# Optimization experiments

Measured on AMD Instinct MI355X. Metric: run time of the kernel, lower is better.

Reference implementation:

```python
import jax, jax.numpy as jnp
import numpy as np

B, D, O, E, H, K = 4096, 1024, 1024, 8, 4096, 2


def setup_inputs() -> dict:
    key = jax.random.key(0)
    ks = jax.random.split(key, 5)
    scale_g = 1.0 / np.sqrt(D)
    scale_1 = 1.0 / np.sqrt(D)
    scale_2 = 1.0 / np.sqrt(H)
    return {
        "x": jax.random.normal(ks[0], (B, D), jnp.float32),
        "gate_w": jax.random.normal(ks[1], (D, E), jnp.float32) * scale_g,
        "gate_b": jnp.zeros((E,), jnp.float32),
        "w1": jax.random.normal(ks[2], (E, D, H), jnp.float32) * scale_1,
        "b1": jnp.zeros((E, H), jnp.float32),
        "w2": jax.random.normal(ks[3], (E, H, O), jnp.float32) * scale_2,
        "b2": jnp.zeros((E, O), jnp.float32),
    }


def reference(x, gate_w, gate_b, w1, b1, w2, b2):
    # Router: top-k logits, softmax over the k selected logits only
    logits = x @ gate_w + gate_b                      # [B, E]
    top_vals, top_idx = jax.lax.top_k(logits, K)      # [B, K]
    routing_w = jax.nn.softmax(top_vals, axis=-1)     # [B, K]

    # Dense all-expert MLP (grouped GEMM), then gather the k selected outputs
    h = jax.nn.relu(jnp.einsum("bd,edh->beh", x, w1) + b1)  # [B, E, H]
    y = jnp.einsum("beh,eho->beo", h, w2) + b2              # [B, E, O]
    sel = jnp.take_along_axis(y, top_idx[:, :, None], axis=1)  # [B, K, O]
    return jnp.sum(routing_w[:, :, None] * sel, axis=1)        # [B, O]
```

## Files before the change

kernel.cpp:

```cpp
#include <hip/hip_runtime.h>
#include <stdint.h>

typedef short bf16x8 __attribute__((ext_vector_type(8)));
typedef float f32x4  __attribute__((ext_vector_type(4)));

constexpr int BT = 4096;
constexpr int DD = 1024;
constexpr int OO = 1024;
constexpr int EE = 8;
constexpr int HH = 4096;
constexpr int SLOTS = 2 * BT;

constexpr int BM = 256, BN = 128, BK = 32;
constexpr int RING = 4;
constexpr int A_USH = BM * BK;
constexpr int TILE_USH = (BM + BN) * BK;
constexpr int MAXT = 40;

__device__ __forceinline__ unsigned short f2bf(float f) {
  unsigned u = __float_as_uint(f);
  u += 0x7fffu + ((u >> 16) & 1u);
  return (unsigned short)(u >> 16);
}

__device__ __forceinline__ void glds16(const unsigned short* g, unsigned short* l) {
  __builtin_amdgcn_global_load_lds(
      (const __attribute__((address_space(1))) void*)g,
      (__attribute__((address_space(3))) void*)l, 16, 0, 0);
}

__global__ __launch_bounds__(256) void router_k(const float* __restrict__ x,
                                                const float* __restrict__ gw,
                                                const float* __restrict__ gb,
                                                unsigned short* __restrict__ xb,
                                                int* __restrict__ cnt,
                                                int* __restrict__ list,
                                                float* __restrict__ rw) {
  int wave = threadIdx.x >> 6, lane = threadIdx.x & 63;
  int b = blockIdx.x * 4 + wave;
  const float* xrow = x + (size_t)b * DD;
  float acc[8];
#pragma unroll
  for (int e = 0; e < 8; ++e) acc[e] = 0.f;
#pragma unroll
  for (int i = 0; i < 4; ++i) {
    int d0 = i * 256 + lane * 4;
    float4 v = *(const float4*)&xrow[d0];
    unsigned lo = (unsigned)f2bf(v.x) | ((unsigned)f2bf(v.y) << 16);
    unsigned hi = (unsigned)f2bf(v.z) | ((unsigned)f2bf(v.w) << 16);
    *(uint2*)&xb[(size_t)b * DD + d0] = make_uint2(lo, hi);
    const float* g0 = &gw[(size_t)d0 * 8];
    float fv[4] = {v.x, v.y, v.z, v.w};
#pragma unroll
    for (int q = 0; q < 4; ++q) {
      float4 ga = *(const float4*)&g0[q * 8];
      float4 gc = *(const float4*)&g0[q * 8 + 4];
      acc[0] += fv[q] * ga.x; acc[1] += fv[q] * ga.y;
      acc[2] += fv[q] * ga.z; acc[3] += fv[q] * ga.w;
      acc[4] += fv[q] * gc.x; acc[5] += fv[q] * gc.y;
      acc[6] += fv[q] * gc.z; acc[7] += fv[q] * gc.w;
    }
  }
#pragma unroll
  for (int off = 32; off > 0; off >>= 1) {
#pragma unroll
    for (int e = 0; e < 8; ++e) acc[e] += __shfl_down(acc[e], off);
  }
  if (lane == 0) {
    float v[8];
#pragma unroll
    for (int e = 0; e < 8; ++e) v[e] = acc[e] + gb[e];
    int i0 = 0;
#pragma unroll
    for (int e = 1; e < 8; ++e) if (v[e] > v[i0]) i0 = e;
    int i1 = (i0 == 0) ? 1 : 0;
#pragma unroll
    for (int e = 0; e < 8; ++e) if (e != i0 && v[e] > v[i1]) i1 = e;
    float e1 = __expf(v[i1] - v[i0]);
    float inv = 1.0f / (1.0f + e1);
    int p0 = atomicAdd(&cnt[i0], 1);
    list[i0 * BT + p0] = 2 * b;     rw[2 * b]     = inv;
    int p1 = atomicAdd(&cnt[i1], 1);
    list[i1 * BT + p1] = 2 * b + 1; rw[2 * b + 1] = e1 * inv;
  }
}

__global__ void tilemap_k(const int* __restrict__ cnt, int* __restrict__ tmap,
                          int* __restrict__ ntiles) {
  if (threadIdx.x == 0 && blockIdx.x == 0) {
    int t = 0, basewalk = 0;
    for (int e = 0; e < EE; ++e) {
      int c = cnt[e];
      for (int m0 = 0; m0 < c; m0 += BM) {
        tmap[4 * t] = e; tmap[4 * t + 1] = m0; tmap[4 * t + 2] = basewalk + m0; ++t;
      }
      basewalk += c;
    }
    *ntiles = t;
  }
}

__global__ __launch_bounds__(256) void cvt_t_k(const float* __restrict__ src,
                                               unsigned short* __restrict__ dst,
                                               int R, int C) {
  __shared__ unsigned short tile[64][66];
  int e = blockIdx.z;
  const float* s = src + (size_t)e * R * C;
  unsigned short* d = dst + (size_t)e * R * C;
  int r0 = blockIdx.x << 6, c0 = blockIdx.y << 6;
  int t = threadIdx.x;
#pragma unroll
  for (int p = 0; p < 4; ++p) {
    int ch = p * 256 + t;
    int rr = ch >> 4, cc = (ch & 15) << 2;
    float4 v = *(const float4*)&s[(size_t)(r0 + rr) * C + c0 + cc];
    unsigned lo = (unsigned)f2bf(v.x) | ((unsigned)f2bf(v.y) << 16);
    unsigned hi = (unsigned)f2bf(v.z) | ((unsigned)f2bf(v.w) << 16);
    *(uint2*)&tile[rr][cc] = make_uint2(lo, hi);
  }
  __syncthreads();
#pragma unroll
  for (int p = 0; p < 4; ++p) {
    int ch = p * 256 + t;
    int cc = ch >> 4, rr = (ch & 15) << 2;
    unsigned short v0 = tile[rr + 0][cc];
    unsigned short v1 = tile[rr + 1][cc];
    unsigned short v2 = tile[rr + 2][cc];
    unsigned short v3 = tile[rr + 3][cc];
    unsigned lo = (unsigned)v0 | ((unsigned)v1 << 16);
    unsigned hi = (unsigned)v2 | ((unsigned)v3 << 16);
    *(uint2*)&d[(size_t)(c0 + cc) * R + r0 + rr] = make_uint2(lo, hi);
  }
}

__global__ __launch_bounds__(512, 2) void gemm1_k(const unsigned short* __restrict__ xb,
                                                  const unsigned short* __restrict__ w1t,
                                                  const float* __restrict__ b1,
                                                  const int* __restrict__ cnt,
                                                  const int* __restrict__ list,
                                                  const int* __restrict__ tmap,
                                                  const int* __restrict__ ntiles,
                                                  unsigned short* __restrict__ hc) {
  int ti = blockIdx.y;
  if (ti >= *ntiles) return;
  int e = tmap[4 * ti], m0 = tmap[4 * ti + 1], base = tmap[4 * ti + 2];
  int cnt_e = cnt[e];
  int n0 = blockIdx.x * BN;

  __shared__ int slotbuf[BM];
  __shared__ __align__(16) unsigned short lds[RING * TILE_USH];

  int t = threadIdx.x;
  if (t < BM) {
    int r = m0 + t;
    slotbuf[t] = list[e * BT + (r < cnt_e ? r : 0)];
  }
  __syncthreads();

  int w = t >> 6, l = t & 63, lm = l & 15, lq = l >> 4;
  int wr = w >> 1, wc = w & 1;

  int rstage = t >> 2;
  int ch8 = (t & 3) * 8;
  const unsigned short* aS0 = xb + (size_t)(slotbuf[rstage] >> 1) * DD + ch8;
  const unsigned short* aS1 = xb + (size_t)(slotbuf[128 + rstage] >> 1) * DD + ch8;
  const unsigned short* bS  = w1t + (size_t)e * HH * DD + (size_t)(n0 + rstage) * DD + ch8;
  int dA0 = w * 512, dA1 = 4096 + w * 512, dB = A_USH + w * 512;

  int afo[4], bfo[4];
#pragma unroll
  for (int mi = 0; mi < 4; ++mi) afo[mi] = (wr * 64 + mi * 16 + lm) * BK + lq * 8;
#pragma unroll
  for (int ni = 0; ni < 4; ++ni) bfo[ni] = A_USH + (wc * 64 + ni * 16 + lm) * BK + lq * 8;

  f32x4 acc[4][4];
#pragma unroll
  for (int mi = 0; mi < 4; ++mi)
#pragma unroll
    for (int ni = 0; ni < 4; ++ni) acc[mi][ni] = f32x4{0.f, 0.f, 0.f, 0.f};

  constexpr int NT = DD / BK;

#pragma unroll
  for (int p = 0; p < RING - 1; ++p) {
    unsigned short* Lb = lds + p * TILE_USH;
    glds16(aS0 + p * BK, Lb + dA0);
    glds16(aS1 + p * BK, Lb + dA1);
    glds16(bS  + p * BK, Lb + dB);
  }
  asm volatile("s_waitcnt vmcnt(6)" ::: "memory");
  __builtin_amdgcn_s_barrier();
  asm volatile("" ::: "memory");

  for (int tt = 0; tt < NT; ++tt) {
    const unsigned short* Lc = lds + (tt & 3) * TILE_USH;
    bf16x8 af[4], bf[4];
#pragma unroll
    for (int mi = 0; mi < 4; ++mi) af[mi] = *(const bf16x8*)&Lc[afo[mi]];
#pragma unroll
    for (int ni = 0; ni < 4; ++ni) bf[ni] = *(const bf16x8*)&Lc[bfo[ni]];
    {
      int ts = tt + 3;
      int ko = (ts < NT ? ts : NT - 1) * BK;
      unsigned short* Lb = lds + (ts & 3) * TILE_USH;
      glds16(aS0 + ko, Lb + dA0);
      glds16(aS1 + ko, Lb + dA1);
      glds16(bS  + ko, Lb + dB);
    }
    __builtin_amdgcn_s_setprio(1);
#pragma unroll
    for (int mi = 0; mi < 4; ++mi)
#pragma unroll
      for (int ni = 0; ni < 4; ++ni)
        acc[mi][ni] = __builtin_amdgcn_mfma_f32_16x16x32_bf16(af[mi], bf[ni], acc[mi][ni], 0, 0, 0);
    __builtin_amdgcn_s_setprio(0);
    asm volatile("s_waitcnt vmcnt(6)" ::: "memory");
    __builtin_amdgcn_s_barrier();
    asm volatile("" ::: "memory");
  }

  asm volatile("s_waitcnt vmcnt(0)" ::: "memory");
  __builtin_amdgcn_s_barrier();
  asm volatile("" ::: "memory");
  unsigned short* cb = lds + w * 4096;
  float bias[4];
#pragma unroll
  for (int ni = 0; ni < 4; ++ni) bias[ni] = b1[e * HH + n0 + wc * 64 + ni * 16 + lm];
#pragma unroll
  for (int mi = 0; mi < 4; ++mi)
#pragma unroll
    for (int ni = 0; ni < 4; ++ni)
#pragma unroll
      for (int r = 0; r < 4; ++r)
        cb[(mi * 16 + lq * 4 + r) * 64 + ni * 16 + lm] =
            f2bf(fmaxf(acc[mi][ni][r] + bias[ni], 0.0f));
  asm volatile("s_waitcnt lgkmcnt(0)" ::: "memory");
#pragma unroll
  for (int it = 0; it < 8; ++it) {
    int rr = it * 8 + (l >> 3), chk = l & 7;
    int lrow = wr * 64 + rr;
    if (m0 + lrow < cnt_e) {
      uint4 v = *(const uint4*)&cb[rr * 64 + chk * 8];
      *(uint4*)&hc[(size_t)(base + lrow) * HH + n0 + wc * 64 + chk * 8] = v;
    }
  }
}

__global__ __launch_bounds__(512, 2) void gemm2_k(const unsigned short* __restrict__ hc,
                                                  const unsigned short* __restrict__ w2t,
                                                  const float* __restrict__ b2,
                                                  const int* __restrict__ cnt,
                                                  const int* __restrict__ list,
                                                  const int* __restrict__ tmap,
                                                  const int* __restrict__ ntiles,
                                                  const float* __restrict__ rw,
                                                  float* __restrict__ ybuf,
                                                  float* __restrict__ out) {
  int ti = blockIdx.y;
  if (ti >= *ntiles) return;
  int e = tmap[4 * ti], m0 = tmap[4 * ti + 1], base = tmap[4 * ti + 2];
  int cnt_e = cnt[e];
  int n0 = blockIdx.x * BN;
  int z = blockIdx.z;
  int ksl = HH / gridDim.z;
  int kb0 = z * ksl;
  int NT = ksl / BK;

  __shared__ int slotbuf[BM];
  __shared__ float rwbuf[BM];
  __shared__ __align__(16) unsigned short lds[RING * TILE_USH];

  int t = threadIdx.x;
  if (t < BM) {
    int r = m0 + t;
    int s_ = list[e * BT + (r < cnt_e ? r : 0)];
    slotbuf[t] = s_;
    rwbuf[t] = rw[s_];
  }
  __syncthreads();

  int w = t >> 6, l = t & 63, lm = l & 15, lq = l >> 4;
  int wr = w >> 1, wc = w & 1;

  int rstage = t >> 2, ch8 = (t & 3) * 8;
  int gr0 = base + rstage;       if (gr0 > SLOTS - 1) gr0 = SLOTS - 1;
  int gr1 = base + 128 + rstage; if (gr1 > SLOTS - 1) gr1 = SLOTS - 1;
  const unsigned short* aS0 = hc + (size_t)gr0 * HH + kb0 + ch8;
  const unsigned short* aS1 = hc + (size_t)gr1 * HH + kb0 + ch8;
  const unsigned short* bS  = w2t + (size_t)e * OO * HH + (size_t)(n0 + rstage) * HH + kb0 + ch8;
  int dA0 = w * 512, dA1 = 4096 + w * 512, dB = A_USH + w * 512;

  int afo[4], bfo[4];
#pragma unroll
  for (int mi = 0; mi < 4; ++mi) afo[mi] = (wr * 64 + mi * 16 + lm) * BK + lq * 8;
#pragma unroll
  for (int ni = 0; ni < 4; ++ni) bfo[ni] = A_USH + (wc * 64 + ni * 16 + lm) * BK + lq * 8;

  f32x4 acc[4][4];
#pragma unroll
  for (int mi = 0; mi < 4; ++mi)
#pragma unroll
    for (int ni = 0; ni < 4; ++ni) acc[mi][ni] = f32x4{0.f, 0.f, 0.f, 0.f};

#pragma unroll
  for (int p = 0; p < RING - 1; ++p) {
    unsigned short* Lb = lds + p * TILE_USH;
    glds16(aS0 + p * BK, Lb + dA0);
    glds16(aS1 + p * BK, Lb + dA1);
    glds16(bS  + p * BK, Lb + dB);
  }
  asm volatile("s_waitcnt vmcnt(6)" ::: "memory");
  __builtin_amdgcn_s_barrier();
  asm volatile("" ::: "memory");

  for (int tt = 0; tt < NT; ++tt) {
    const unsigned short* Lc = lds + (tt & 3) * TILE_USH;
    bf16x8 af[4], bf[4];
#pragma unroll
    for (int mi = 0; mi < 4; ++mi) af[mi] = *(const bf16x8*)&Lc[afo[mi]];
#pragma unroll
    for (int ni = 0; ni < 4; ++ni) bf[ni] = *(const bf16x8*)&Lc[bfo[ni]];
    {
      int ts = tt + 3;
      int ko = (ts < NT ? ts : NT - 1) * BK;
      unsigned short* Lb = lds + (ts & 3) * TILE_USH;
      glds16(aS0 + ko, Lb + dA0);
      glds16(aS1 + ko, Lb + dA1);
      glds16(bS  + ko, Lb + dB);
    }
    __builtin_amdgcn_s_setprio(1);
#pragma unroll
    for (int mi = 0; mi < 4; ++mi)
#pragma unroll
      for (int ni = 0; ni < 4; ++ni)
        acc[mi][ni] = __builtin_amdgcn_mfma_f32_16x16x32_bf16(af[mi], bf[ni], acc[mi][ni], 0, 0, 0);
    __builtin_amdgcn_s_setprio(0);
    asm volatile("s_waitcnt vmcnt(6)" ::: "memory");
    __builtin_amdgcn_s_barrier();
    asm volatile("" ::: "memory");
  }

  bool addb = (z == 0);
  size_t ybase = (size_t)z * SLOTS;
#pragma unroll
  for (int ni = 0; ni < 4; ++ni) {
    int ncol = n0 + wc * 64 + ni * 16 + lm;
    float bias = addb ? b2[e * OO + ncol] : 0.0f;
#pragma unroll
    for (int mi = 0; mi < 4; ++mi)
#pragma unroll
      for (int r = 0; r < 4; ++r) {
        int lrow = wr * 64 + mi * 16 + lq * 4 + r;
        if (m0 + lrow < cnt_e) {
          float v = (acc[mi][ni][r] + bias) * rwbuf[lrow];
          int slot = slotbuf[lrow];
          if (ybuf) ybuf[(ybase + slot) * OO + ncol] = v;
          else      atomicAdd(&out[(size_t)(slot >> 1) * OO + ncol], v);
        }
      }
  }
}

__global__ __launch_bounds__(256) void combine_k(const float* __restrict__ y,
                                                 float* __restrict__ out, int nz) {
  int i = blockIdx.x * 256 + threadIdx.x;
  int b = i >> 8, c = i & 255;
  f32x4 acc = {0.f, 0.f, 0.f, 0.f};
  for (int z = 0; z < nz; ++z) {
#pragma unroll
    for (int k = 0; k < 2; ++k) {
      const float4 v = *(const float4*)&y[((size_t)z * SLOTS + 2 * b + k) * OO + c * 4];
      acc[0] += v.x; acc[1] += v.y; acc[2] += v.z; acc[3] += v.w;
    }
  }
  *(f32x4*)&out[(size_t)b * OO + c * 4] = acc;
}

extern "C" void kernel_launch(void* const* d_in, const int* in_sizes, int n_in,
                              void* d_out, int out_size, void* d_ws, size_t ws_size,
                              hipStream_t stream) {
  const float* x  = (const float*)d_in[0];
  const float* gw = (const float*)d_in[1];
  const float* gb = (const float*)d_in[2];
  const float* w1 = (const float*)d_in[3];
  const float* b1 = (const float*)d_in[4];
  const float* w2 = (const float*)d_in[5];
  const float* b2 = (const float*)d_in[6];
  float* out = (float*)d_out;
  char* ws = (char*)d_ws;

  int*            cnt    = (int*)(ws);
  int*            ntiles = (int*)(ws + 64);
  int*            tmap   = (int*)(ws + 128);
  float*          rw     = (float*)(ws + 4096);
  int*            list   = (int*)(ws + (64u << 10));
  unsigned short* xb     = (unsigned short*)(ws + (1u  << 20));
  unsigned short* wt     = (unsigned short*)(ws + (9u  << 20));
  unsigned short* hc     = (unsigned short*)(ws + (73u << 20));
  float*          ybuf   = (float*)(ws + (138u << 20));

  size_t need_min = (138u << 20);
  if (ws_size < need_min) return;
  int zsplit;
  float* ypass;
  if (ws_size >= (138u << 20) + (size_t)2 * SLOTS * OO * 4) { zsplit = 2; ypass = ybuf; }
  else if (ws_size >= (138u << 20) + (size_t)SLOTS * OO * 4) { zsplit = 1; ypass = ybuf; }
  else { zsplit = 2; ypass = nullptr; }

  hipMemsetAsync(cnt, 0, 64, stream);
  if (!ypass) hipMemsetAsync(out, 0, (size_t)BT * OO * sizeof(float), stream);

  router_k<<<BT / 4, 256, 0, stream>>>(x, gw, gb, xb, cnt, list, rw);
  tilemap_k<<<1, 64, 0, stream>>>(cnt, tmap, ntiles);
  cvt_t_k<<<dim3(DD / 64, HH / 64, EE), 256, 0, stream>>>(w1, wt, DD, HH);
  gemm1_k<<<dim3(HH / BN, MAXT), 512, 0, stream>>>(xb, wt, b1, cnt, list, tmap, ntiles, hc);
  cvt_t_k<<<dim3(HH / 64, OO / 64, EE), 256, 0, stream>>>(w2, wt, HH, OO);
  gemm2_k<<<dim3(OO / BN, MAXT, zsplit), 512, 0, stream>>>(hc, wt, b2, cnt, list, tmap, ntiles, rw, ypass, out);
  if (ypass)
    combine_k<<<BT * OO / 1024, 256, 0, stream>>>(ybuf, out, zsplit);
}
```

Baseline: 683.2 us.

## Widen GEMM tiles to 256x256 with XOR-swizzled LDS and reordered prefetch

Both grouped GEMM kernels grow the N tile from 128 to 256, so each warp now computes a 128x64 sub-tile (8x4 MFMAs) in a 2x4 warp grid. This raises arithmetic intensity per LDS byte and per global load. LDS chunks are XOR-swizzled on both the global_load_lds write side and the fragment read side to cut bank conflicts, and the next-stage prefetch is now issued before the fragment reads. The cost is higher register pressure from 128 accumulator floats per lane, larger LDS use, and fewer blocks in the grid. Host launch grid dimensions presumably have to change for the wider tile, and that part is not shown.

Result: slower. 733.8 us (+7.4%).

```diff
diff --git a/kernel.cpp b/kernel.cpp
--- a/kernel.cpp
+++ b/kernel.cpp
@@ -11,10 +11,10 @@
 constexpr int HH = 4096;
 constexpr int SLOTS = 2 * BT;
 
-constexpr int BM = 256, BN = 128, BK = 32;
+constexpr int BM = 256, BN = 256, BK = 32;
 constexpr int RING = 4;
 constexpr int A_USH = BM * BK;
-constexpr int TILE_USH = (BM + BN) * BK;
+constexpr int SLOT_USH = (BM + BN) * BK;
 constexpr int MAXT = 40;
 
 __device__ __forceinline__ unsigned short f2bf(float f) {
@@ -148,7 +148,7 @@
   int n0 = blockIdx.x * BN;
 
   __shared__ int slotbuf[BM];
-  __shared__ __align__(16) unsigned short lds[RING * TILE_USH];
+  __shared__ __align__(16) unsigned short lds[RING * SLOT_USH];
 
   int t = threadIdx.x;
   if (t < BM) {
@@ -158,24 +158,31 @@
   __syncthreads();
 
   int w = t >> 6, l = t & 63, lm = l & 15, lq = l >> 4;
-  int wr = w >> 1, wc = w & 1;
-
-  int rstage = t >> 2;
-  int ch8 = (t & 3) * 8;
-  const unsigned short* aS0 = xb + (size_t)(slotbuf[rstage] >> 1) * DD + ch8;
-  const unsigned short* aS1 = xb + (size_t)(slotbuf[128 + rstage] >> 1) * DD + ch8;
-  const unsigned short* bS  = w1t + (size_t)e * HH * DD + (size_t)(n0 + rstage) * DD + ch8;
-  int dA0 = w * 512, dA1 = 4096 + w * 512, dB = A_USH + w * 512;
-
-  int afo[4], bfo[4];
-#pragma unroll
-  for (int mi = 0; mi < 4; ++mi) afo[mi] = (wr * 64 + mi * 16 + lm) * BK + lq * 8;
-#pragma unroll
-  for (int ni = 0; ni < 4; ++ni) bfo[ni] = A_USH + (wc * 64 + ni * 16 + lm) * BK + lq * 8;
-
-  f32x4 acc[4][4];
-#pragma unroll
-  for (int mi = 0; mi < 4; ++mi)
+  int wr = w >> 2, wc = w & 3;
+
+  const unsigned short* aS[2];
+  const unsigned short* bS[2];
+  int dA[2], dB[2];
+#pragma unroll
+  for (int j = 0; j < 2; ++j) {
+    int row = j * 128 + w * 16 + (l >> 2);
+    int sch = ((l & 3) ^ ((row >> 1) & 3)) * 8;
+    aS[j] = xb + (size_t)(slotbuf[row] >> 1) * DD + sch;
+    bS[j] = w1t + (size_t)e * HH * DD + (size_t)(n0 + row) * DD + sch;
+    dA[j] = j * 4096 + w * 512;
+    dB[j] = A_USH + j * 4096 + w * 512;
+  }
+
+  int xc = lq ^ ((lm >> 1) & 3);
+  int afo[8], bfo[4];
+#pragma unroll
+  for (int mi = 0; mi < 8; ++mi) afo[mi] = (wr * 128 + mi * 16 + lm) * BK + xc * 8;
+#pragma unroll
+  for (int ni = 0; ni < 4; ++ni) bfo[ni] = A_USH + (wc * 64 + ni * 16 + lm) * BK + xc * 8;
+
+  f32x4 acc[8][4];
+#pragma unroll
+  for (int mi = 0; mi < 8; ++mi)
 #pragma unroll
     for (int ni = 0; ni < 4; ++ni) acc[mi][ni] = f32x4{0.f, 0.f, 0.f, 0.f};
 
@@ -183,38 +190,40 @@
 
 #pragma unroll
   for (int p = 0; p < RING - 1; ++p) {
-    unsigned short* Lb = lds + p * TILE_USH;
-    glds16(aS0 + p * BK, Lb + dA0);
-    glds16(aS1 + p * BK, Lb + dA1);
-    glds16(bS  + p * BK, Lb + dB);
-  }
-  asm volatile("s_waitcnt vmcnt(6)" ::: "memory");
+    unsigned short* Lb = lds + p * SLOT_USH;
+    glds16(aS[0] + p * BK, Lb + dA[0]);
+    glds16(aS[1] + p * BK, Lb + dA[1]);
+    glds16(bS[0] + p * BK, Lb + dB[0]);
+    glds16(bS[1] + p * BK, Lb + dB[1]);
+  }
+  asm volatile("s_waitcnt vmcnt(8)" ::: "memory");
   __builtin_amdgcn_s_barrier();
   asm volatile("" ::: "memory");
 
   for (int tt = 0; tt < NT; ++tt) {
-    const unsigned short* Lc = lds + (tt & 3) * TILE_USH;
-    bf16x8 af[4], bf[4];
-#pragma unroll
-    for (int mi = 0; mi < 4; ++mi) af[mi] = *(const bf16x8*)&Lc[afo[mi]];
-#pragma unroll
-    for (int ni = 0; ni < 4; ++ni) bf[ni] = *(const bf16x8*)&Lc[bfo[ni]];
     {
       int ts = tt + 3;
       int ko = (ts < NT ? ts : NT - 1) * BK;
-      unsigned short* Lb = lds + (ts & 3) * TILE_USH;
-      glds16(aS0 + ko, Lb + dA0);
-      glds16(aS1 + ko, Lb + dA1);
-      glds16(bS  + ko, Lb + dB);
-    }
+      unsigned short* Lb = lds + (ts & 3) * SLOT_USH;
+      glds16(aS[0] + ko, Lb + dA[0]);
+      glds16(aS[1] + ko, Lb + dA[1]);
+      glds16(bS[0] + ko, Lb + dB[0]);
+      glds16(bS[1] + ko, Lb + dB[1]);
+    }
+    const unsigned short* Lc = lds + (tt & 3) * SLOT_USH;
+    bf16x8 af[8], bf[4];
+#pragma unroll
+    for (int mi = 0; mi < 8; ++mi) af[mi] = *(const bf16x8*)&Lc[afo[mi]];
+#pragma unroll
+    for (int ni = 0; ni < 4; ++ni) bf[ni] = *(const bf16x8*)&Lc[bfo[ni]];
     __builtin_amdgcn_s_setprio(1);
 #pragma unroll
-    for (int mi = 0; mi < 4; ++mi)
+    for (int mi = 0; mi < 8; ++mi)
 #pragma unroll
       for (int ni = 0; ni < 4; ++ni)
         acc[mi][ni] = __builtin_amdgcn_mfma_f32_16x16x32_bf16(af[mi], bf[ni], acc[mi][ni], 0, 0, 0);
     __builtin_amdgcn_s_setprio(0);
-    asm volatile("s_waitcnt vmcnt(6)" ::: "memory");
+    asm volatile("s_waitcnt vmcnt(8)" ::: "memory");
     __builtin_amdgcn_s_barrier();
     asm volatile("" ::: "memory");
   }
@@ -222,12 +231,12 @@
   asm volatile("s_waitcnt vmcnt(0)" ::: "memory");
   __builtin_amdgcn_s_barrier();
   asm volatile("" ::: "memory");
-  unsigned short* cb = lds + w * 4096;
+  unsigned short* cb = lds + w * 8192;
   float bias[4];
 #pragma unroll
   for (int ni = 0; ni < 4; ++ni) bias[ni] = b1[e * HH + n0 + wc * 64 + ni * 16 + lm];
 #pragma unroll
-  for (int mi = 0; mi < 4; ++mi)
+  for (int mi = 0; mi < 8; ++mi)
 #pragma unroll
     for (int ni = 0; ni < 4; ++ni)
 #pragma unroll
@@ -236,12 +245,12 @@
             f2bf(fmaxf(acc[mi][ni][r] + bias[ni], 0.0f));
   asm volatile("s_waitcnt lgkmcnt(0)" ::: "memory");
 #pragma unroll
-  for (int it = 0; it < 8; ++it) {
+  for (int it = 0; it < 16; ++it) {
     int rr = it * 8 + (l >> 3), chk = l & 7;
-    int lrow = wr * 64 + rr;
-    if (m0 + lrow < cnt_e) {
+    int grow = wr * 128 + rr;
+    if (m0 + grow < cnt_e) {
       uint4 v = *(const uint4*)&cb[rr * 64 + chk * 8];
-      *(uint4*)&hc[(size_t)(base + lrow) * HH + n0 + wc * 64 + chk * 8] = v;
+      *(uint4*)&hc[(size_t)(base + grow) * HH + n0 + wc * 64 + chk * 8] = v;
     }
   }
 }
@@ -268,7 +277,7 @@
 
   __shared__ int slotbuf[BM];
   __shared__ float rwbuf[BM];
-  __shared__ __align__(16) unsigned short lds[RING * TILE_USH];
+  __shared__ __align__(16) unsigned short lds[RING * SLOT_USH];
 
   int t = threadIdx.x;
   if (t < BM) {
@@ -280,65 +289,75 @@
   __syncthreads();
 
   int w = t >> 6, l = t & 63, lm = l & 15, lq = l >> 4;
-  int wr = w >> 1, wc = w & 1;
-
-  int rstage = t >> 2, ch8 = (t & 3) * 8;
-  int gr0 = base + rstage;       if (gr0 > SLOTS - 1) gr0 = SLOTS - 1;
-  int gr1 = base + 128 + rstage; if (gr1 > SLOTS - 1) gr1 = SLOTS - 1;
-  const unsigned short* aS0 = hc + (size_t)gr0 * HH + kb0 + ch8;
-  const unsigned short* aS1 = hc + (size_t)gr1 * HH + kb0 + ch8;
-  const unsigned short* bS  = w2t + (size_t)e * OO * HH + (size_t)(n0 + rstage) * HH + kb0 + ch8;
-  int dA0 = w * 512, dA1 = 4096 + w * 512, dB = A_USH + w * 512;
-
-  int afo[4], bfo[4];
-#pragma unroll
-  for (int mi = 0; mi < 4; ++mi) afo[mi] = (wr * 64 + mi * 16 + lm) * BK + lq * 8;
-#pragma unroll
-  for (int ni = 0; ni < 4; ++ni) bfo[ni] = A_USH + (wc * 64 + ni * 16 + lm) * BK + lq * 8;
-
-  f32x4 acc[4][4];
-#pragma unroll
-  for (int mi = 0; mi < 4; ++mi)
+  int wr = w >> 2, wc = w & 3;
+
+  const unsigned short* aS[2];
+  const unsigned short* bS[2];
+  int dA[2], dB[2];
+#pragma unroll
+  for (int j = 0; j < 2; ++j) {
+    int row = j * 128 + w * 16 + (l >> 2);
+    int sch = ((l & 3) ^ ((row >> 1) & 3)) * 8;
+    int gr = base + row; if (gr > SLOTS - 1) gr = SLOTS - 1;
+    aS[j] = hc + (size_t)gr * HH + kb0 + sch;
+    bS[j] = w2t + (size_t)e * OO * HH + (size_t)(n0 + row) * HH + kb0 + sch;
+    dA[j] = j * 4096 + w * 512;
+    dB[j] = A_USH + j * 4096 + w * 512;
+  }
+
+  int xc = lq ^ ((lm >> 1) & 3);
+  int afo[8], bfo[4];
+#pragma unroll
+  for (int mi = 0; mi < 8; ++mi) afo[mi] = (wr * 128 + mi * 16 + lm) * BK + xc * 8;
+#pragma unroll
+  for (int ni = 0; ni < 4; ++ni) bfo[ni] = A_USH + (wc * 64 + ni * 16 + lm) * BK + xc * 8;
+
+  f32x4 acc[8][4];
+#pragma unroll
+  for (int mi = 0; mi < 8; ++mi)
 #pragma unroll
     for (int ni = 0; ni < 4; ++ni) acc[mi][ni] = f32x4{0.f, 0.f, 0.f, 0.f};
 
 #pragma unroll
   for (int p = 0; p < RING - 1; ++p) {
-    unsigned short* Lb = lds + p * TILE_USH;
-    glds16(aS0 + p * BK, Lb + dA0);
-    glds16(aS1 + p * BK, Lb + dA1);
-    glds16(bS  + p * BK, Lb + dB);
-  }
-  asm volatile("s_waitcnt vmcnt(6)" ::: "memory");
+    unsigned short* Lb = lds + p * SLOT_USH;
+    glds16(aS[0] + p * BK, Lb + dA[0]);
+    glds16(aS[1] + p * BK, Lb + dA[1]);
+    glds16(bS[0] + p * BK, Lb + dB[0]);
+    glds16(bS[1] + p * BK, Lb + dB[1]);
+  }
+  asm volatile("s_waitcnt vmcnt(8)" ::: "memory");
   __builtin_amdgcn_s_barrier();
   asm volatile("" ::: "memory");
 
   for (int tt = 0; tt < NT; ++tt) {
-    const unsigned short* Lc = lds + (tt & 3) * TILE_USH;
-    bf16x8 af[4], bf[4];
-#pragma unroll
-    for (int mi = 0; mi < 4; ++mi) af[mi] = *(const bf16x8*)&Lc[afo[mi]];
-#pragma unroll
-    for (int ni = 0; ni < 4; ++ni) bf[ni] = *(const bf16x8*)&Lc[bfo[ni]];
     {
       int ts = tt + 3;
       int ko = (ts < NT ? ts : NT - 1) * BK;
-      unsigned short* Lb = lds + (ts & 3) * TILE_USH;
-      glds16(aS0 + ko, Lb + dA0);
-      glds16(aS1 + ko, Lb + dA1);
-      glds16(bS  + ko, Lb + dB);
-    }
+      unsigned short* Lb = lds + (ts & 3) * SLOT_USH;
+      glds16(aS[0] + ko, Lb + dA[0]);
+      glds16(aS[1] + ko, Lb + dA[1]);
+      glds16(bS[0] + ko, Lb + dB[0]);
+      glds16(bS[1] + ko, Lb + dB[1]);
+    }
+    const unsigned short* Lc = lds + (tt & 3) * SLOT_USH;
+    bf16x8 af[8], bf[4];
+#pragma unroll
+    for (int mi = 0; mi < 8; ++mi) af[mi] = *(const bf16x8*)&Lc[afo[mi]];
+#pragma unroll
+    for (int ni = 0; ni < 4; ++ni) bf[ni] = *(const bf16x8*)&Lc[bfo[ni]];
     __builtin_amdgcn_s_setprio(1);
 #pragma unroll
-    for (int mi = 0; mi < 4; ++mi)
+    for (int mi = 0; mi < 8; ++mi)
 #pragma unroll
       for (int ni = 0; ni < 4; ++ni)
         acc[mi][ni] = __builtin_amdgcn_mfma_f32_16x16x32_bf16(af[mi], bf[ni], acc[mi][ni], 0, 0, 0);
     __builtin_amdgcn_s_setprio(0);
-    asm volatile("s_waitcnt vmcnt(6)" ::: "memory");
+    asm volatile("s_waitcnt vmcnt(8)" ::: "memory");
     __builtin_amdgcn_s_barrier();
     asm volatile("" ::: "memory");
   }
+  asm volatile("s_waitcnt vmcnt(0)" ::: "memory");
 
   bool addb = (z == 0);
   size_t ybase = (size_t)z * SLOTS;
@@ -347,10 +366,10 @@
     int ncol = n0 + wc * 64 + ni * 16 + lm;
     float bias = addb ? b2[e * OO + ncol] : 0.0f;
 #pragma unroll
-    for (int mi = 0; mi < 4; ++mi)
+    for (int mi = 0; mi < 8; ++mi)
 #pragma unroll
       for (int r = 0; r < 4; ++r) {
-        int lrow = wr * 64 + mi * 16 + lq * 4 + r;
+        int lrow = wr * 128 + mi * 16 + lq * 4 + r;
         if (m0 + lrow < cnt_e) {
           float v = (acc[mi][ni][r] + bias) * rwbuf[lrow];
           int slot = slotbuf[lrow];
```
